# Optimization experiments

Hardware: AMD Instinct MI355X
Metric: run time of the kernel (lower is better)

Reference implementation:

```python
import jax, jax.numpy as jnp
import numpy as np

D_OUT, D1, D2 = 512, 512, 512
R0, R1, R2 = 128, 128, 128
BATCH = 8192


def setup_inputs() -> dict:
    key = jax.random.key(0)
    k1, k2, k3, k4, k5, k6 = jax.random.split(key, 6)
    return {
        "X1": jax.random.normal(k1, (D1, BATCH), dtype=jnp.float32),
        "X2": jax.random.normal(k2, (D2, BATCH), dtype=jnp.float32),
        "U0": jax.random.normal(k3, (D_OUT, R0), dtype=jnp.float32) * 0.05,
        "U1": jax.random.normal(k4, (D1, R1), dtype=jnp.float32) * 0.05,
        "U2": jax.random.normal(k5, (D2, R2), dtype=jnp.float32) * 0.05,
        "G": jax.random.normal(k6, (R0, R1, R2), dtype=jnp.float32) * 0.05,
    }


def reference(X1, X2, U0, U1, U2, G):
    # Per-mode projections: UX_i = U_{i+1}^T @ X_i  -> [r_i, B]
    UX1 = U1.T @ X1  # [R1, B]
    UX2 = U2.T @ X2  # [R2, B]
    # Column-wise Khatri-Rao product of UX1, UX2 gives kron per column with
    # row index q*R2 + r (C order), which matches mode-0 unfolding of G.
    # Fused form: core = G_(0) @ khatri_rao(UX1, UX2), expressed as one einsum.
    core = jnp.einsum('pqr,qb,rb->pb', G, UX1, UX2)  # [R0, B]
    Z = U0 @ core  # [D_OUT, B]
    return Z
```

## Files before the change

kernel.cpp:

```cpp
#include <hip/hip_runtime.h>
#include <hip/hip_bf16.h>
#include <stdint.h>


typedef __attribute__((ext_vector_type(8))) short bf8;
typedef __attribute__((ext_vector_type(4))) short bf4;
typedef __attribute__((ext_vector_type(4))) float f4;

__device__ __forceinline__ unsigned short f2bf(float f){
  unsigned x = __builtin_bit_cast(unsigned, f);
  x += 0x7fffu + ((x >> 16) & 1u);
  return (unsigned short)(x >> 16);
}
__device__ __forceinline__ float bf2f(unsigned short u){
  unsigned x = ((unsigned)u) << 16;
  return __builtin_bit_cast(float, x);
}
__device__ __forceinline__ void glds16(const void* g, void* l){
  __builtin_amdgcn_global_load_lds(
      (const __attribute__((address_space(1))) void*)g,
      (__attribute__((address_space(3))) void*)l, 16, 0, 0);
}

__global__ __launch_bounds__(256) void k_cast(const float* __restrict__ G,
                                              const float* __restrict__ U0,
                                              const float* __restrict__ U1,
                                              const float* __restrict__ U2,
                                              unsigned short* __restrict__ Gbf,
                                              unsigned short* __restrict__ U0bf,
                                              unsigned short* __restrict__ U1T,
                                              unsigned short* __restrict__ U2T){
  const int blk = blockIdx.x;
  if (blk < 2112){
    const int i4 = blk * 256 + threadIdx.x;
    const int NG4 = 2097152 / 4;
    const float4* src; unsigned short* dst; int j4;
    if (i4 < NG4){ src = (const float4*)G;  dst = Gbf;  j4 = i4; }
    else         { src = (const float4*)U0; dst = U0bf; j4 = i4 - NG4; }
    float4 v = src[j4];
    ushort4 o = make_ushort4(f2bf(v.x), f2bf(v.y), f2bf(v.z), f2bf(v.w));
    ((ushort4*)dst)[j4] = o;
  } else {
    const int b2 = blk - 2112;
    const float* U = (b2 < 256) ? U1 : U2;
    unsigned short* UT = (b2 < 256) ? U1T : U2T;
    const int idx = (b2 & 255) * 256 + threadIdx.x;
    const int d = idx >> 7, q = idx & 127;
    UT[q * 512 + d] = f2bf(U[idx]);
  }
}

__global__ __launch_bounds__(256) void k_ux2(const unsigned short* __restrict__ U1T,
                                             const unsigned short* __restrict__ U2T,
                                             const float* __restrict__ X1,
                                             const float* __restrict__ X2,
                                             float* __restrict__ OUTF,
                                             unsigned short* __restrict__ OUTT){
  const bool second = (blockIdx.y != 0);
  const unsigned short* UT = second ? U2T : U1T;
  const float* X = second ? X2 : X1;
  __shared__ __align__(16) unsigned char lds[16384 + 8192];
  unsigned char* ldsA = lds;
  unsigned char* ldsB = lds + 16384;
  const int tid = threadIdx.x, lane = tid & 63, wv = tid >> 6;
  const int wr = wv >> 1, wc = wv & 1;
  const int b0 = blockIdx.x * 64;
  f4 acc[4][2] = {};

  for (int it = 0; it < 8; ++it){
    const int k0 = it * 64;
#pragma unroll
    for (int i = 0; i < 4; ++i){
      const int L = (wv * 4 + i) * 1024 + lane * 16;
      const int row = L >> 7;
      const int ss = (lane & 7) ^ (row & 7);
      glds16(UT + (size_t)row * 512 + k0 + ss * 8, ldsA + (wv * 4 + i) * 1024);
    }
#pragma unroll
    for (int c = 0; c < 2; ++c){
      const int slot = c * 4 + wv;
      const int bRow = lane;
      bf8 v;
#pragma unroll
      for (int j = 0; j < 8; ++j)
        v[j] = (short)f2bf(X[(size_t)(k0 + slot * 8 + j) * 8192 + b0 + bRow]);
      *(bf8*)(ldsB + bRow * 128 + ((slot ^ (bRow & 7)) << 4)) = v;
    }
    __syncthreads();
#pragma unroll
    for (int kc = 0; kc < 2; ++kc){
      const int g = lane >> 4;
      bf8 a[4], b[2];
#pragma unroll
      for (int mf = 0; mf < 4; ++mf){
        const int r = wr * 64 + mf * 16 + (lane & 15);
        a[mf] = *(const bf8*)(ldsA + r * 128 + (((kc * 4 + g) ^ (r & 7)) << 4));
      }
#pragma unroll
      for (int nf = 0; nf < 2; ++nf){
        const int rb = wc * 32 + nf * 16 + (lane & 15);
        b[nf] = *(const bf8*)(ldsB + rb * 128 + (((kc * 4 + g) ^ (rb & 7)) << 4));
      }
#pragma unroll
      for (int mf = 0; mf < 4; ++mf)
#pragma unroll
        for (int nf = 0; nf < 2; ++nf)
          acc[mf][nf] = __builtin_amdgcn_mfma_f32_16x16x32_bf16(a[mf], b[nf], acc[mf][nf], 0, 0, 0);
    }
    __syncthreads();
  }

  if (!second){
#pragma unroll
    for (int mf = 0; mf < 4; ++mf)
#pragma unroll
      for (int nf = 0; nf < 2; ++nf)
#pragma unroll
        for (int j = 0; j < 4; ++j){
          const int q = wr * 64 + mf * 16 + (lane >> 4) * 4 + j;
          const int b = b0 + wc * 32 + nf * 16 + (lane & 15);
          OUTF[(size_t)q * 8192 + b] = acc[mf][nf][j];
        }
  } else {
#pragma unroll
    for (int mf = 0; mf < 4; ++mf)
#pragma unroll
      for (int nf = 0; nf < 2; ++nf){
        const int rBase = wr * 64 + mf * 16 + (lane >> 4) * 4;
        const int bL = wc * 32 + nf * 16 + (lane & 15);
        bf4 p;
#pragma unroll
        for (int j = 0; j < 4; ++j) p[j] = (short)f2bf(acc[mf][nf][j]);
        *(bf4*)(lds + ((bL * 256 + rBase * 2) ^ ((bL & 7) << 4))) = p;
      }
    __syncthreads();
#pragma unroll
    for (int u = 0; u < 4; ++u){
      const int sIdx = u * 256 + tid;
      const int bL = sIdx >> 4, slot = sIdx & 15;
      bf8 v = *(const bf8*)(lds + bL * 256 + ((slot ^ (bL & 7)) << 4));
      *(bf8*)(OUTT + (size_t)(b0 + bL) * 128 + slot * 8) = v;
    }
  }
}

__global__ __launch_bounds__(512, 2) void k_core(const unsigned short* __restrict__ Gbf,
                                                 const float* __restrict__ UX1,
                                                 const unsigned short* __restrict__ UX2T,
                                                 unsigned short* __restrict__ PT){
  __shared__ __align__(16) unsigned char lds[114688];
  unsigned char* ldsX = lds + 98304;
  const int tid = threadIdx.x, lane = tid & 63, wv = tid >> 6;
  const int g = lane >> 4, l15 = lane & 15;
  const int wr = wv >> 2, wc = wv & 3;
  const int blk = blockIdx.x;
  const int split = blk & 7;
  const int b0 = (blk >> 3) * 256;
  const int q0 = split * 16;

  auto stageA = [&](int q, int buf, int rnd){
    const int off = rnd * 8192 + wv * 1024 + lane * 16;
    const int row = off >> 8;
    const int ss = ((off >> 4) & 15) ^ (row & 7);
    glds16(Gbf + (size_t)row * 16384 + (size_t)q * 128 + ss * 8,
           lds + buf * 32768 + off);
  };

  bf8 Bf[4][4];
#pragma unroll
  for (int kc = 0; kc < 4; ++kc)
#pragma unroll
    for (int nf = 0; nf < 4; ++nf)
      Bf[kc][nf] = *(const bf8*)(UX2T + (size_t)(b0 + wc * 64 + nf * 16 + l15) * 128 +
                                 kc * 32 + g * 8);
#pragma unroll
  for (int rnd = 0; rnd < 2; ++rnd){
    const int off = rnd * 8192 + wv * 1024 + lane * 16;
    const int row = off >> 10;
    glds16(UX1 + (size_t)(q0 + row) * 8192 + b0 + ((off >> 2) & 255), ldsX + off);
  }
#pragma unroll
  for (int rnd = 0; rnd < 4; ++rnd) stageA(q0, 0, rnd);
#pragma unroll
  for (int rnd = 0; rnd < 4; ++rnd) stageA(q0 + 1, 1, rnd);

  f4 acc[4][4];
#pragma unroll
  for (int mf = 0; mf < 4; ++mf)
#pragma unroll
    for (int nf = 0; nf < 4; ++nf) acc[mf][nf] = (f4){0.f, 0.f, 0.f, 0.f};
  float xs[4];

  asm volatile("s_waitcnt vmcnt(4)" ::: "memory");
  __builtin_amdgcn_s_barrier();

  auto phase = [&](int i, const unsigned char* A, int ph, bool doStage,
                   int stq, int sbuf, int vm){
    bf8 a[2][4];
#pragma unroll
    for (int mfp = 0; mfp < 2; ++mfp){
      const int row = wr * 64 + (ph * 2 + mfp) * 16 + l15;
#pragma unroll
      for (int kc = 0; kc < 4; ++kc)
        a[mfp][kc] = *(const bf8*)(A + row * 256 + ((((kc << 2) + g) ^ (row & 7)) << 4));
    }
    if (ph == 0){
#pragma unroll
      for (int nf = 0; nf < 4; ++nf)
        xs[nf] = *(const float*)(ldsX + i * 1024 + (wc * 64 + nf * 16 + l15) * 4);
    }
    if (doStage){ stageA(stq, sbuf, ph * 2); stageA(stq, sbuf, ph * 2 + 1); }
    __builtin_amdgcn_s_barrier();
    asm volatile("s_waitcnt lgkmcnt(0)" ::: "memory");
    __builtin_amdgcn_sched_barrier(0);
    __builtin_amdgcn_s_setprio(1);
    f4 y[2][4];
#pragma unroll
    for (int mfp = 0; mfp < 2; ++mfp)
#pragma unroll
      for (int nf = 0; nf < 4; ++nf){
        f4 t = __builtin_amdgcn_mfma_f32_16x16x32_bf16(a[mfp][0], Bf[0][nf], (f4){0.f,0.f,0.f,0.f}, 0, 0, 0);
        t = __builtin_amdgcn_mfma_f32_16x16x32_bf16(a[mfp][1], Bf[1][nf], t, 0, 0, 0);
        t = __builtin_amdgcn_mfma_f32_16x16x32_bf16(a[mfp][2], Bf[2][nf], t, 0, 0, 0);
        y[mfp][nf] = __builtin_amdgcn_mfma_f32_16x16x32_bf16(a[mfp][3], Bf[3][nf], t, 0, 0, 0);
      }
    __builtin_amdgcn_s_setprio(0);
#pragma unroll
    for (int mfp = 0; mfp < 2; ++mfp)
#pragma unroll
      for (int nf = 0; nf < 4; ++nf)
        acc[ph * 2 + mfp][nf] += y[mfp][nf] * xs[nf];
    if (vm == 4)      asm volatile("s_waitcnt vmcnt(4)" ::: "memory");
    else if (vm == 0) asm volatile("s_waitcnt vmcnt(0)" ::: "memory");
    __builtin_amdgcn_s_barrier();
  };

  int cur = 0;
  for (int i = 0; i < 14; ++i){
    const unsigned char* A = lds + cur * 32768;
    int sbuf = cur + 2; if (sbuf >= 3) sbuf -= 3;
    phase(i, A, 0, true, q0 + i + 2, sbuf, -1);
    phase(i, A, 1, true, q0 + i + 2, sbuf, 4);
    ++cur; if (cur == 3) cur = 0;
  }
  {
    const unsigned char* A = lds + cur * 32768;
    phase(14, A, 0, false, 0, 0, -1);
    phase(14, A, 1, false, 0, 0, 0);
    ++cur; if (cur == 3) cur = 0;
  }
  {
    const unsigned char* A = lds + cur * 32768;
    phase(15, A, 0, false, 0, 0, -1);
    phase(15, A, 1, false, 0, 0, -1);
  }

  __syncthreads();
#pragma unroll
  for (int mf = 0; mf < 4; ++mf)
#pragma unroll
    for (int nf = 0; nf < 4; ++nf){
      const int bL = wc * 64 + nf * 16 + l15;
      const int pq = wr * 16 + mf * 4 + g;
      bf4 o;
#pragma unroll
      for (int j = 0; j < 4; ++j) o[j] = (short)f2bf(acc[mf][nf][j]);
      *(bf4*)(lds + bL * 256 + ((pq ^ (bL & 7)) << 3)) = o;
    }
  __syncthreads();
#pragma unroll
  for (int rnd = 0; rnd < 8; ++rnd){
    const int idx = rnd * 512 + tid;
    const int bL = idx >> 4, s8 = idx & 15;
    bf4 lo = *(const bf4*)(lds + bL * 256 + (((s8 * 2) ^ (bL & 7)) << 3));
    bf4 hi = *(const bf4*)(lds + bL * 256 + (((s8 * 2 + 1) ^ (bL & 7)) << 3));
    bf8 o;
#pragma unroll
    for (int j = 0; j < 4; ++j){ o[j] = lo[j]; o[4 + j] = hi[j]; }
    *(bf8*)(PT + (size_t)split * 1048576 + (size_t)(b0 + bL) * 128 + s8 * 8) = o;
  }
}

__global__ __launch_bounds__(256) void k_red(const unsigned short* __restrict__ PT,
                                             unsigned short* __restrict__ coreT){
  const int c = blockIdx.x * 256 + threadIdx.x;
  const bf8* P = (const bf8*)PT;
  float s[8] = {};
#pragma unroll
  for (int sp = 0; sp < 8; ++sp){
    bf8 v = P[c + sp * 131072];
#pragma unroll
    for (int j = 0; j < 8; ++j) s[j] += bf2f((unsigned short)v[j]);
  }
  bf8 o;
#pragma unroll
  for (int j = 0; j < 8; ++j) o[j] = (short)f2bf(s[j]);
  ((bf8*)coreT)[c] = o;
}

__global__ __launch_bounds__(256) void k_z(const unsigned short* __restrict__ U0bf,
                                           const unsigned short* __restrict__ coreT,
                                           float* __restrict__ Z){
  __shared__ __align__(16) unsigned char lds[32768];
  unsigned char* ldsA = lds;
  unsigned char* ldsB = lds + 16384;
  const int tid = threadIdx.x, lane = tid & 63, wv = tid >> 6;
  const int wr = wv >> 1, wc = wv & 1;
  const int b0 = blockIdx.x * 128;
  const int d0 = blockIdx.y * 128;
  f4 acc[4][4] = {};

#pragma unroll
  for (int it = 0; it < 2; ++it){
    const int k0 = it * 64;
#pragma unroll
    for (int i = 0; i < 4; ++i){
      const int L = (wv * 4 + i) * 1024 + lane * 16;
      const int row = L >> 7;
      const int ss = (lane & 7) ^ (row & 7);
      glds16(U0bf + (size_t)(d0 + row) * 128 + k0 + ss * 8, ldsA + (wv * 4 + i) * 1024);
      glds16(coreT + (size_t)(b0 + row) * 128 + k0 + ss * 8, ldsB + (wv * 4 + i) * 1024);
    }
    __syncthreads();
#pragma unroll
    for (int kc = 0; kc < 2; ++kc){
      const int g = lane >> 4;
      bf8 a[4], b[4];
#pragma unroll
      for (int mf = 0; mf < 4; ++mf){
        const int r = wr * 64 + mf * 16 + (lane & 15);
        a[mf] = *(const bf8*)(ldsA + r * 128 + (((kc * 4 + g) ^ (r & 7)) << 4));
      }
#pragma unroll
      for (int nf = 0; nf < 4; ++nf){
        const int rb = wc * 64 + nf * 16 + (lane & 15);
        b[nf] = *(const bf8*)(ldsB + rb * 128 + (((kc * 4 + g) ^ (rb & 7)) << 4));
      }
#pragma unroll
      for (int mf = 0; mf < 4; ++mf)
#pragma unroll
        for (int nf = 0; nf < 4; ++nf)
          acc[mf][nf] = __builtin_amdgcn_mfma_f32_16x16x32_bf16(a[mf], b[nf], acc[mf][nf], 0, 0, 0);
    }
    __syncthreads();
  }
#pragma unroll
  for (int mf = 0; mf < 4; ++mf)
#pragma unroll
    for (int nf = 0; nf < 4; ++nf)
#pragma unroll
      for (int j = 0; j < 4; ++j){
        const int d = d0 + wr * 64 + mf * 16 + (lane >> 4) * 4 + j;
        const int b = b0 + wc * 64 + nf * 16 + (lane & 15);
        Z[(size_t)d * 8192 + b] = acc[mf][nf][j];
      }
}

extern "C" void kernel_launch(void* const* d_in, const int* in_sizes, int n_in,
                              void* d_out, int out_size, void* d_ws, size_t ws_size,
                              hipStream_t stream){
  const float* X1 = (const float*)d_in[0];
  const float* X2 = (const float*)d_in[1];
  const float* U0 = (const float*)d_in[2];
  const float* U1 = (const float*)d_in[3];
  const float* U2 = (const float*)d_in[4];
  const float* G  = (const float*)d_in[5];
  float* Z = (float*)d_out;

  char* ws = (char*)d_ws;
  unsigned short* Gbf   = (unsigned short*)(ws);
  unsigned short* U0bf  = (unsigned short*)(ws + 4194304);
  unsigned short* U1T   = (unsigned short*)(ws + 4325376);
  unsigned short* U2T   = (unsigned short*)(ws + 4456448);
  float*          UX1   = (float*)         (ws + 4587520);
  unsigned short* UX2T  = (unsigned short*)(ws + 8781824);
  unsigned short* coreT = (unsigned short*)(ws + 10878976);
  unsigned short* PT    = (unsigned short*)(ws + 12976128);

  k_cast<<<dim3(2624), dim3(256), 0, stream>>>(G, U0, U1, U2, Gbf, U0bf, U1T, U2T);
  k_ux2 <<<dim3(128, 2), dim3(256), 0, stream>>>(U1T, U2T, X1, X2, UX1, UX2T);
  k_core<<<dim3(256), dim3(512), 0, stream>>>(Gbf, UX1, UX2T, PT);
  k_red <<<dim3(512), dim3(256), 0, stream>>>(PT, coreT);
  k_z   <<<dim3(64, 4), dim3(256), 0, stream>>>(U0bf, coreT, Z);
}
```

Baseline: 71.11 us.

## Simplify core-kernel pipeline to one barrier per iteration with full-tile staging

Replaces the hand-scheduled two-phase-per-iteration loop with one loop over all 16 q slices. Each iteration does a single wait and barrier, then issues all four G-tile async loads for slice i+2 into the triple buffer, then computes all four M fragments. This removes three of the four barriers per slice, along with the explicit sched_barrier and setprio control. The interleaving of LDS reads and MFMAs is now left to the compiler. The risk is poorer overlap or more register pressure from the looser instruction scheduling.

```diff
diff --git a/kernel.cpp b/kernel.cpp
--- a/kernel.cpp
+++ b/kernel.cpp
@@ -158,12 +158,15 @@
   const int b0 = (blk >> 3) * 256;
   const int q0 = split * 16;
 
-  auto stageA = [&](int q, int buf, int rnd){
-    const int off = rnd * 8192 + wv * 1024 + lane * 16;
-    const int row = off >> 8;
-    const int ss = ((off >> 4) & 15) ^ (row & 7);
-    glds16(Gbf + (size_t)row * 16384 + (size_t)q * 128 + ss * 8,
-           lds + buf * 32768 + off);
+  auto stageA = [&](int q, int buf){
+#pragma unroll
+    for (int rnd = 0; rnd < 4; ++rnd){
+      const int off = rnd * 8192 + wv * 1024 + lane * 16;
+      const int row = off >> 8;
+      const int ss = ((off >> 4) & 15) ^ (row & 7);
+      glds16(Gbf + (size_t)row * 16384 + (size_t)q * 128 + ss * 8,
+             lds + buf * 32768 + off);
+    }
   };
 
   bf8 Bf[4][4];
@@ -179,80 +182,47 @@
     const int row = off >> 10;
     glds16(UX1 + (size_t)(q0 + row) * 8192 + b0 + ((off >> 2) & 255), ldsX + off);
   }
-#pragma unroll
-  for (int rnd = 0; rnd < 4; ++rnd) stageA(q0, 0, rnd);
-#pragma unroll
-  for (int rnd = 0; rnd < 4; ++rnd) stageA(q0 + 1, 1, rnd);
+  stageA(q0 + 0, 0);
+  stageA(q0 + 1, 1);
 
   f4 acc[4][4];
 #pragma unroll
   for (int mf = 0; mf < 4; ++mf)
 #pragma unroll
     for (int nf = 0; nf < 4; ++nf) acc[mf][nf] = (f4){0.f, 0.f, 0.f, 0.f};
-  float xs[4];
-
-  asm volatile("s_waitcnt vmcnt(4)" ::: "memory");
-  __builtin_amdgcn_s_barrier();
-
-  auto phase = [&](int i, const unsigned char* A, int ph, bool doStage,
-                   int stq, int sbuf, int vm){
-    bf8 a[2][4];
-#pragma unroll
-    for (int mfp = 0; mfp < 2; ++mfp){
-      const int row = wr * 64 + (ph * 2 + mfp) * 16 + l15;
+
+  int cur = 0;
+  for (int i = 0; i < 16; ++i){
+    if (i < 15) asm volatile("s_waitcnt vmcnt(4)" ::: "memory");
+    else        asm volatile("s_waitcnt vmcnt(0)" ::: "memory");
+    __builtin_amdgcn_s_barrier();
+    if (i < 14){
+      int sbuf = cur + 2; if (sbuf >= 3) sbuf -= 3;
+      stageA(q0 + i + 2, sbuf);
+    }
+
+    const unsigned char* A = lds + cur * 32768;
+    float xs[4];
+#pragma unroll
+    for (int nf = 0; nf < 4; ++nf)
+      xs[nf] = *(const float*)(ldsX + i * 1024 + (wc * 64 + nf * 16 + l15) * 4);
+#pragma unroll
+    for (int mf = 0; mf < 4; ++mf){
+      const int row = wr * 64 + mf * 16 + l15;
+      bf8 a[4];
 #pragma unroll
       for (int kc = 0; kc < 4; ++kc)
-        a[mfp][kc] = *(const bf8*)(A + row * 256 + ((((kc << 2) + g) ^ (row & 7)) << 4));
-    }
-    if (ph == 0){
-#pragma unroll
-      for (int nf = 0; nf < 4; ++nf)
-        xs[nf] = *(const float*)(ldsX + i * 1024 + (wc * 64 + nf * 16 + l15) * 4);
-    }
-    if (doStage){ stageA(stq, sbuf, ph * 2); stageA(stq, sbuf, ph * 2 + 1); }
-    __builtin_amdgcn_s_barrier();
-    asm volatile("s_waitcnt lgkmcnt(0)" ::: "memory");
-    __builtin_amdgcn_sched_barrier(0);
-    __builtin_amdgcn_s_setprio(1);
-    f4 y[2][4];
-#pragma unroll
-    for (int mfp = 0; mfp < 2; ++mfp)
+        a[kc] = *(const bf8*)(A + row * 256 + ((((kc << 2) + g) ^ (row & 7)) << 4));
 #pragma unroll
       for (int nf = 0; nf < 4; ++nf){
-        f4 t = __builtin_amdgcn_mfma_f32_16x16x32_bf16(a[mfp][0], Bf[0][nf], (f4){0.f,0.f,0.f,0.f}, 0, 0, 0);
-        t = __builtin_amdgcn_mfma_f32_16x16x32_bf16(a[mfp][1], Bf[1][nf], t, 0, 0, 0);
-        t = __builtin_amdgcn_mfma_f32_16x16x32_bf16(a[mfp][2], Bf[2][nf], t, 0, 0, 0);
-        y[mfp][nf] = __builtin_amdgcn_mfma_f32_16x16x32_bf16(a[mfp][3], Bf[3][nf], t, 0, 0, 0);
-      }
-    __builtin_amdgcn_s_setprio(0);
-#pragma unroll
-    for (int mfp = 0; mfp < 2; ++mfp)
-#pragma unroll
-      for (int nf = 0; nf < 4; ++nf)
-        acc[ph * 2 + mfp][nf] += y[mfp][nf] * xs[nf];
-    if (vm == 4)      asm volatile("s_waitcnt vmcnt(4)" ::: "memory");
-    else if (vm == 0) asm volatile("s_waitcnt vmcnt(0)" ::: "memory");
-    __builtin_amdgcn_s_barrier();
-  };
-
-  int cur = 0;
-  for (int i = 0; i < 14; ++i){
-    const unsigned char* A = lds + cur * 32768;
-    int sbuf = cur + 2; if (sbuf >= 3) sbuf -= 3;
-    phase(i, A, 0, true, q0 + i + 2, sbuf, -1);
-    phase(i, A, 1, true, q0 + i + 2, sbuf, 4);
+        f4 y = __builtin_amdgcn_mfma_f32_16x16x32_bf16(a[0], Bf[0][nf], (f4){0.f,0.f,0.f,0.f}, 0, 0, 0);
+        y = __builtin_amdgcn_mfma_f32_16x16x32_bf16(a[1], Bf[1][nf], y, 0, 0, 0);
+        y = __builtin_amdgcn_mfma_f32_16x16x32_bf16(a[2], Bf[2][nf], y, 0, 0, 0);
+        y = __builtin_amdgcn_mfma_f32_16x16x32_bf16(a[3], Bf[3][nf], y, 0, 0, 0);
+        acc[mf][nf] += y * xs[nf];
+      }
+    }
     ++cur; if (cur == 3) cur = 0;
-  }
-  {
-    const unsigned char* A = lds + cur * 32768;
-    phase(14, A, 0, false, 0, 0, -1);
-    phase(14, A, 1, false, 0, 0, 0);
-    ++cur; if (cur == 3) cur = 0;
-  }
-  {
-    const unsigned char* A = lds + cur * 32768;
-    phase(15, A, 0, false, 0, 0, -1);
-    phase(15, A, 1, false, 0, 0, -1);
   }
 
   __syncthreads();
```

New measurement: 69.11 us. -2.8%, faster.
